# Kernel tuning notes

Hardware: AMD Instinct MI355X
Metric: run time of the kernel (lower is better)

## Reference

```python
import jax, jax.numpy as jnp
import numpy as np

B, S, D = 2, 2048, 2048
NH, NKV = 32, 8
HD = D // NH           # 64
GS = NH // NKV         # 4
ROPE_BASE = 10000.0


def _rope_tables(seq_len, head_dim, base):
    inv_freq = 1.0 / (base ** (jnp.arange(head_dim // 2, dtype=jnp.float32) / (head_dim // 2)))
    angles = jnp.arange(seq_len, dtype=jnp.float32)[:, None] * inv_freq[None, :]  # [S, HD/2]
    angles = jnp.concatenate([angles, angles], axis=-1)                            # [S, HD]
    return jnp.cos(angles), jnp.sin(angles)


def _apply_rope(x, cos, sin):
    # x: [B, H, S, HD]
    hd = x.shape[-1]
    x1, x2 = x[..., : hd // 2], x[..., hd // 2 :]
    rotated = jnp.concatenate([-x2, x1], axis=-1)
    return (x * cos[None, None] + rotated * sin[None, None]).astype(x.dtype)


def setup_inputs() -> dict:
    key = jax.random.key(0)
    ks = jax.random.split(key, 5)
    scale = 0.02
    return {
        "x": jax.random.normal(ks[0], (B, S, D), dtype=jnp.float32),
        "Wq": jax.random.normal(ks[1], (D, D), dtype=jnp.float32) * scale,
        "Wk": jax.random.normal(ks[2], (D, NKV * HD), dtype=jnp.float32) * scale,
        "Wv": jax.random.normal(ks[3], (D, NKV * HD), dtype=jnp.float32) * scale,
        "Wo": jax.random.normal(ks[4], (D, D), dtype=jnp.float32) * scale,
    }


def reference(x, Wq, Wk, Wv, Wo):
    b, n, _ = x.shape
    cos, sin = _rope_tables(n, HD, ROPE_BASE)

    q = (x @ Wq).reshape(b, n, NH, HD).transpose(0, 2, 1, 3)    # [B, NH, S, HD]
    k = (x @ Wk).reshape(b, n, NKV, HD).transpose(0, 2, 1, 3)   # [B, NKV, S, HD]
    v = (x @ Wv).reshape(b, n, NKV, HD).transpose(0, 2, 1, 3)

    q = _apply_rope(q, cos, sin)
    k = _apply_rope(k, cos, sin)

    # GQA head sharing: repeat_interleave KV groups to full head count
    k = jnp.repeat(k, GS, axis=1)   # [B, NH, S, HD]
    v = jnp.repeat(v, GS, axis=1)

    scores = jnp.einsum("bhqd,bhkd->bhqk", q, k)                # [B, NH, S, S]
    causal = jnp.triu(jnp.ones((n, n), dtype=bool), k=1)
    scores = jnp.where(causal[None, None], -jnp.inf, scores)
    weights = jax.nn.softmax(scores / jnp.sqrt(jnp.float32(HD)), axis=-1)

    ctx = jnp.einsum("bhqk,bhkd->bhqd", weights, v)             # [B, NH, S, HD]
    ctx = ctx.transpose(0, 2, 1, 3).reshape(b, n, D)
    return ctx @ Wo
```

## Files before the change

kernel.cpp:

```cpp
#include <hip/hip_runtime.h>

typedef __bf16 bf16;
typedef __attribute__((ext_vector_type(8))) __bf16 bf16x8;
typedef __attribute__((ext_vector_type(4))) float f32x4;
typedef __attribute__((ext_vector_type(4))) short s16x4;

#define S_LEN 2048
#define D_MODEL 2048
#define NHEADS 32
#define NKVH 8
#define HDIM 64
#define BATCH 2

__device__ __forceinline__ void async_cp16(const bf16* g, bf16* l) {
    __builtin_amdgcn_global_load_lds(
        (const __attribute__((address_space(1))) unsigned int*)g,
        (__attribute__((address_space(3))) unsigned int*)l, 16, 0, 0);
}

__global__ void preproc(const float* __restrict__ x,
                        const float* __restrict__ Wq, const float* __restrict__ Wk,
                        const float* __restrict__ Wv, const float* __restrict__ Wo,
                        bf16* __restrict__ X16, bf16* __restrict__ WqT, bf16* __restrict__ WkT,
                        bf16* __restrict__ WvT, bf16* __restrict__ WoT) {
    __shared__ float tile[32][33];
    const int tid = threadIdx.x;
    int bid = blockIdx.x;
    if (bid < 8192) {
        int i = bid * 256 + tid;
        float4 f = ((const float4*)x)[i];
        union { bf16 h[4]; uint2 u; } t;
        t.h[0] = (bf16)f.x; t.h[1] = (bf16)f.y; t.h[2] = (bf16)f.z; t.h[3] = (bf16)f.w;
        ((uint2*)X16)[i] = t.u;
        return;
    }
    int l = bid - 8192;
    const float* W; bf16* Wt; int N, bx, by;
    const int K = 2048;
    if (l < 4096)      {            W = Wq; Wt = WqT; N = 2048; bx = l & 63; by = l >> 6; }
    else if (l < 5120) { l -= 4096; W = Wk; Wt = WkT; N = 512;  bx = l & 15; by = l >> 4; }
    else if (l < 6144) { l -= 5120; W = Wv; Wt = WvT; N = 512;  bx = l & 15; by = l >> 4; }
    else               { l -= 6144; W = Wo; Wt = WoT; N = 2048; bx = l & 63; by = l >> 6; }
    const int kt = by * 32, nt = bx * 32;
    const int tx = tid & 31, ty = tid >> 5;
    #pragma unroll
    for (int i = 0; i < 32; i += 8)
        tile[ty + i][tx] = W[(size_t)(kt + ty + i) * N + nt + tx];
    __syncthreads();
    #pragma unroll
    for (int i = 0; i < 32; i += 8)
        Wt[(size_t)(nt + ty + i) * K + kt + tx] = (bf16)tile[tx][ty + i];
}

template <bool OUT_BF16>
__global__ __launch_bounds__(256) void gemm_bt(const bf16* __restrict__ A,
                                               const bf16* __restrict__ Bt,
                                               void* __restrict__ Cv,
                                               int M, int N, int K) {
    __shared__ __align__(16) bf16 As[128 * 64];
    __shared__ __align__(16) bf16 Bs[128 * 64];

    const int tid  = threadIdx.x;
    const int wave = tid >> 6;
    const int lane = tid & 63;
    const int l16  = lane & 15;
    const int quad = lane >> 4;
    const int wrow = (wave >> 1) * 64;
    const int wcol = (wave & 1) * 64;
    const int m0 = blockIdx.y * 128;
    const int n0 = blockIdx.x * 128;

    const int krow = lane >> 3;
    const int kc   = (lane & 7) ^ krow;
    const bf16* gA = A  + (size_t)(m0 + wave * 32 + krow) * K + kc * 8;
    const bf16* gB = Bt + (size_t)(n0 + wave * 32 + krow) * K + kc * 8;
    bf16* lA = &As[wave * 2048];
    bf16* lB = &Bs[wave * 2048];
    const size_t rstep = (size_t)8 * K;

    const int sw = l16 & 7;

    f32x4 acc[4][4];
    #pragma unroll
    for (int mi = 0; mi < 4; ++mi)
        #pragma unroll
        for (int ni = 0; ni < 4; ++ni)
            acc[mi][ni] = (f32x4){0.f, 0.f, 0.f, 0.f};

    for (int k0 = 0; k0 < K; k0 += 64) {
        __syncthreads();
        async_cp16(gA,             lA);
        async_cp16(gA +     rstep, lA + 512);
        async_cp16(gA + 2 * rstep, lA + 1024);
        async_cp16(gA + 3 * rstep, lA + 1536);
        async_cp16(gB,             lB);
        async_cp16(gB +     rstep, lB + 512);
        async_cp16(gB + 2 * rstep, lB + 1024);
        async_cp16(gB + 3 * rstep, lB + 1536);
        gA += 64; gB += 64;
        __syncthreads();

        #pragma unroll
        for (int kk = 0; kk < 2; ++kk) {
            bf16x8 af[4], bfr[4];
            #pragma unroll
            for (int mi = 0; mi < 4; ++mi)
                af[mi] = *(const bf16x8*)&As[(wrow + mi * 16 + l16) * 64 + (((kk * 4 + quad) ^ sw) * 8)];
            #pragma unroll
            for (int ni = 0; ni < 4; ++ni)
                bfr[ni] = *(const bf16x8*)&Bs[(wcol + ni * 16 + l16) * 64 + (((kk * 4 + quad) ^ sw) * 8)];
            #pragma unroll
            for (int mi = 0; mi < 4; ++mi)
                #pragma unroll
                for (int ni = 0; ni < 4; ++ni)
                    acc[mi][ni] = __builtin_amdgcn_mfma_f32_16x16x32_bf16(af[mi], bfr[ni], acc[mi][ni], 0, 0, 0);
        }
    }

    #pragma unroll
    for (int mi = 0; mi < 4; ++mi) {
        #pragma unroll
        for (int ni = 0; ni < 4; ++ni) {
            #pragma unroll
            for (int r = 0; r < 4; ++r) {
                size_t row = (size_t)(m0 + wrow + mi * 16 + quad * 4 + r);
                size_t col = (size_t)(n0 + wcol + ni * 16 + l16);
                if (OUT_BF16) ((bf16*)Cv)[row * N + col] = (bf16)acc[mi][ni][r];
                else          ((float*)Cv)[row * N + col] = acc[mi][ni][r];
            }
        }
    }
}

#define BUF1 16384

#define VMW(n) asm volatile("s_waitcnt vmcnt(" #n ")" ::: "memory")
#define BAR __builtin_amdgcn_s_barrier()

#define STAGE_A0(BUFOFF) do { \
    async_cp16(pa00, As + (BUFOFF) + la00); \
    async_cp16(pa01, As + (BUFOFF) + la01); \
    pa00 += 64; pa01 += 64; } while (0)
#define STAGE_A1(BUFOFF) do { \
    async_cp16(pa10, As + (BUFOFF) + la10); \
    async_cp16(pa11, As + (BUFOFF) + la11); \
    pa10 += 64; pa11 += 64; } while (0)
#define STAGE_B0(BUFOFF) do { \
    async_cp16(pb00, Bs + (BUFOFF) + lb00); \
    async_cp16(pb01, Bs + (BUFOFF) + lb01); \
    pb00 += 64; pb01 += 64; } while (0)
#define STAGE_B1(BUFOFF) do { \
    async_cp16(pb10, Bs + (BUFOFF) + lb10); \
    async_cp16(pb11, Bs + (BUFOFF) + lb11); \
    pb10 += 64; pb11 += 64; } while (0)

#define READ_A(QM, BUFOFF) do { \
    _Pragma("unroll") \
    for (int m_ = 0; m_ < 4; ++m_) { \
        const int row_ = wr * 128 + (QM) * 64 + m_ * 16 + l16; \
        af[m_][0] = *(const bf16x8*)&As[(BUFOFF) + row_ * 64 + ((quad ^ sw8) * 8)]; \
        af[m_][1] = *(const bf16x8*)&As[(BUFOFF) + row_ * 64 + (((4 + quad) ^ sw8) * 8)]; \
    } } while (0)

#define READ_B(QN, BUFOFF, BV) do { \
    _Pragma("unroll") \
    for (int n_ = 0; n_ < 2; ++n_) { \
        const int row_ = wc * 64 + (QN) * 32 + n_ * 16 + l16; \
        BV[n_][0] = *(const bf16x8*)&Bs[(BUFOFF) + row_ * 64 + ((quad ^ sw8) * 8)]; \
        BV[n_][1] = *(const bf16x8*)&Bs[(BUFOFF) + row_ * 64 + (((4 + quad) ^ sw8) * 8)]; \
    } } while (0)

#define MFMA_Q(QM, QN, BV) do { \
    _Pragma("unroll") \
    for (int kk_ = 0; kk_ < 2; ++kk_) \
        _Pragma("unroll") \
        for (int m_ = 0; m_ < 4; ++m_) \
            _Pragma("unroll") \
            for (int n_ = 0; n_ < 2; ++n_) \
                acc[(QM) * 4 + m_][(QN) * 2 + n_] = __builtin_amdgcn_mfma_f32_16x16x32_bf16( \
                    af[m_][kk_], BV[n_][kk_], acc[(QM) * 4 + m_][(QN) * 2 + n_], 0, 0, 0); \
    } while (0)

#define SYNCM(QM, QN, BV) do { \
    BAR; \
    __builtin_amdgcn_s_setprio(1); \
    MFMA_Q(QM, QN, BV); \
    __builtin_amdgcn_s_setprio(0); } while (0)

#define TILE_S(CUR) do { \
    READ_A(0, CUR); READ_B(0, CUR, bfr0);             SYNCM(0, 0, bfr0); BAR; \
    STAGE_A0(CUR); STAGE_B0(CUR); READ_B(1, CUR, bfr1); SYNCM(0, 1, bfr1); BAR; \
    STAGE_B1(CUR); READ_A(1, CUR);                    SYNCM(1, 0, bfr0); BAR; \
    STAGE_A1(CUR);                                    SYNCM(1, 1, bfr1); VMW(8); BAR; } while (0)

#define TILE_N(CUR, W) do { \
    READ_A(0, CUR); READ_B(0, CUR, bfr0); SYNCM(0, 0, bfr0); BAR; \
    READ_B(1, CUR, bfr1);                 SYNCM(0, 1, bfr1); BAR; \
    READ_A(1, CUR);                       SYNCM(1, 0, bfr0); BAR; \
                                          SYNCM(1, 1, bfr1); W; BAR; } while (0)

template <bool OUT_BF16>
__global__ __launch_bounds__(512, 2) void gemm256(const bf16* __restrict__ A,
                                                  const bf16* __restrict__ Bt,
                                                  void* __restrict__ Cv,
                                                  int N, int K) {
    __shared__ __align__(16) bf16 As[2 * 256 * 64];
    __shared__ __align__(16) bf16 Bs[2 * 256 * 64];

    const int tid  = threadIdx.x;
    const int w    = tid >> 6;
    const int lane = tid & 63;
    const int l16  = lane & 15;
    const int quad = lane >> 4;
    const int sw8  = l16 & 7;
    const int wr   = w >> 2;
    const int wc   = w & 3;

    const int nbx  = N >> 8;
    const int nwg  = gridDim.x;
    const int orig = blockIdx.x;
    const int wg   = (orig & 7) * (nwg >> 3) + (orig >> 3);
    const int n0   = (wg % nbx) * 256;
    const int m0   = (wg / nbx) * 256;

    const int krow = lane >> 3;
    const int kc   = (lane & 7) ^ krow;

    const bf16* pa00 = A + (size_t)(m0 +   0 + w * 8 + krow) * K + kc * 8;
    const bf16* pa01 = A + (size_t)(m0 + 128 + w * 8 + krow) * K + kc * 8;
    const bf16* pa10 = A + (size_t)(m0 +  64 + w * 8 + krow) * K + kc * 8;
    const bf16* pa11 = A + (size_t)(m0 + 192 + w * 8 + krow) * K + kc * 8;
    const int brow0 = (w >> 2) * 64 + (w & 3) * 8 + krow;
    const bf16* pb00 = Bt + (size_t)(n0 +       brow0) * K + kc * 8;
    const bf16* pb01 = Bt + (size_t)(n0 + 128 + brow0) * K + kc * 8;
    const bf16* pb10 = Bt + (size_t)(n0 +  32 + brow0) * K + kc * 8;
    const bf16* pb11 = Bt + (size_t)(n0 + 160 + brow0) * K + kc * 8;

    const int la00 = w * 512;
    const int la01 = 8192 + w * 512;
    const int la10 = 4096 + w * 512;
    const int la11 = 12288 + w * 512;
    const int lbb  = ((w >> 2) * 64 + (w & 3) * 8) * 64;
    const int lb00 = lbb;
    const int lb01 = 8192 + lbb;
    const int lb10 = 2048 + lbb;
    const int lb11 = 10240 + lbb;

    f32x4 acc[8][4];
    #pragma unroll
    for (int i = 0; i < 8; ++i)
        #pragma unroll
        for (int j = 0; j < 4; ++j) acc[i][j] = (f32x4){0.f, 0.f, 0.f, 0.f};

    bf16x8 af[4][2];
    bf16x8 bfr0[2][2];
    bf16x8 bfr1[2][2];

    STAGE_A0(0); STAGE_B0(0); STAGE_B1(0); STAGE_A1(0);
    STAGE_A0(BUF1); STAGE_B0(BUF1); STAGE_B1(BUF1); STAGE_A1(BUF1);
    VMW(8);
    BAR;

    const int NITER = K >> 6;
    for (int it = 0; it < (NITER - 2) >> 1; ++it) {
        TILE_S(0);
        TILE_S(BUF1);
    }
    TILE_N(0, VMW(0));
    TILE_N(BUF1, );

    #pragma unroll
    for (int mi = 0; mi < 8; ++mi)
        #pragma unroll
        for (int ni = 0; ni < 4; ++ni)
            #pragma unroll
            for (int r = 0; r < 4; ++r) {
                size_t row = (size_t)(m0 + wr * 128 + mi * 16 + quad * 4 + r);
                size_t col = (size_t)(n0 + wc * 64 + ni * 16 + l16);
                if (OUT_BF16) ((bf16*)Cv)[row * N + col] = (bf16)acc[mi][ni][r];
                else          ((float*)Cv)[row * N + col] = acc[mi][ni][r];
            }
}

__global__ void rope_tv(const bf16* __restrict__ QKV,
                        bf16* __restrict__ Qr, bf16* __restrict__ Kr,
                        bf16* __restrict__ Vt) {
    __shared__ bf16 tl[32][33];
    const int tid = threadIdx.x;
    const int bid = blockIdx.x;
    const float LC = 0.28782313662425572f;
    const float QS = 0.18033688011112042f;
    if (bid < 20480) {
        const int QN = BATCH * S_LEN * NHEADS * 32;
        int idx = bid * 256 + tid;
        if (idx < QN) {
            int j = idx & 31, hh = (idx >> 5) & 31, s = (idx >> 10) & 2047, bb = idx >> 21;
            size_t src = ((size_t)(bb * S_LEN + s)) * 3072 + hh * HDIM + j;
            float x1 = (float)QKV[src], x2 = (float)QKV[src + 32];
            float ang = (float)s * __expf(-(float)j * LC);
            float sn, cs; sincosf(ang, &sn, &cs);
            size_t dst = ((size_t)((bb * NHEADS + hh) * S_LEN + s)) * HDIM + j;
            Qr[dst]      = (bf16)((x1 * cs - x2 * sn) * QS);
            Qr[dst + 32] = (bf16)((x2 * cs + x1 * sn) * QS);
        } else {
            int t = idx - QN;
            int j = t & 31, hh = (t >> 5) & 7, s = (t >> 8) & 2047, bb = t >> 19;
            size_t src = ((size_t)(bb * S_LEN + s)) * 3072 + 2048 + hh * HDIM + j;
            float x1 = (float)QKV[src], x2 = (float)QKV[src + 32];
            float ang = (float)s * __expf(-(float)j * LC);
            float sn, cs; sincosf(ang, &sn, &cs);
            size_t dst = ((size_t)((bb * NKVH + hh) * S_LEN + s)) * HDIM + j;
            Kr[dst]      = (bf16)(x1 * cs - x2 * sn);
            Kr[dst + 32] = (bf16)(x2 * cs + x1 * sn);
        }
        return;
    }
    int l = bid - 20480;
    int s0 = (l & 63) * 32;
    int d0 = ((l >> 6) & 1) * 32;
    int z  = l >> 7;
    int bb = z >> 3, hh = z & 7;
    int tx = tid & 31, ty = tid >> 5;
    #pragma unroll
    for (int i = 0; i < 32; i += 8)
        tl[ty + i][tx] = QKV[((size_t)(bb * S_LEN + s0 + ty + i)) * 3072 + 2560 + hh * 64 + d0 + tx];
    __syncthreads();
    #pragma unroll
    for (int i = 0; i < 32; i += 8)
        Vt[((size_t)z * 64 + d0 + ty + i) * S_LEN + s0 + tx] = tl[tx][ty + i];
}

__global__ __launch_bounds__(256, 3) void attn_kernel(const bf16* __restrict__ Q,
                                                      const bf16* __restrict__ K,
                                                      const bf16* __restrict__ Vt,
                                                      bf16* __restrict__ Ctx) {
    __shared__ __align__(16) bf16 KsL[128 * 64];
    __shared__ __align__(16) bf16 VtL[64 * 128];

    static const signed char QTAB[16] = {15,14,13,12, 10,11,8,9, 5,4,7,6, 0,1,2,3};
    const int bx = blockIdx.x;
    const int qt = QTAB[((bx >> 8) << 2) | ((bx >> 6) & 3)];
    const int bh = bx & 63;
    const int b  = bh >> 5;
    const int h  = bh & 31;
    const int kvh = h >> 2;
    const int tid = threadIdx.x;
    const int wave = tid >> 6;
    const int lane = tid & 63;
    const int l16  = lane & 15;
    const int quad = lane >> 4;

    const bf16* Qb = Q  + ((size_t)(b * NHEADS + h)) * S_LEN * HDIM;
    const bf16* Kb = K  + ((size_t)(b * NKVH + kvh)) * S_LEN * HDIM;
    const bf16* Vb = Vt + ((size_t)(b * NKVH + kvh)) * HDIM * S_LEN;

    const int q0 = qt * 128;

    bf16x8 aq[2][2];
    #pragma unroll
    for (int qf = 0; qf < 2; ++qf)
        #pragma unroll
        for (int ks = 0; ks < 2; ++ks)
            aq[qf][ks] = *(const bf16x8*)(Qb + (size_t)(q0 + wave * 32 + qf * 16 + l16) * HDIM + ks * 32 + quad * 8);

    f32x4 O[2][4];
    float M0 = -1e30f, M1 = -1e30f;
    float l0 = 0.f, l1 = 0.f;
    #pragma unroll
    for (int qf = 0; qf < 2; ++qf)
        #pragma unroll
        for (int df = 0; df < 4; ++df) O[qf][df] = (f32x4){0.f,0.f,0.f,0.f};

    const int krow = lane >> 3, kslot = lane & 7;
    const int kc   = kslot ^ (krow & 7);
    const int vslot = lane & 15, vsub = lane >> 4;

    #pragma unroll 1
    for (int kt = 0; kt <= qt; ++kt) {
        const int k0 = kt * 128;
        __syncthreads();
        #pragma unroll
        for (int j = 0; j < 4; ++j) {
            int rbase = (wave * 4 + j) * 8;
            async_cp16(Kb + (size_t)(k0 + rbase + krow) * HDIM + kc * 8, &KsL[rbase * 64]);
            int d0 = (wave * 4 + j) * 4;
            int vrow = d0 + vsub;
            int vc = vslot ^ (vrow & 15);
            async_cp16(Vb + (size_t)vrow * S_LEN + k0 + vc * 8, &VtL[d0 * 128]);
        }
        __syncthreads();

        f32x4 sc[2][8];
        #pragma unroll
        for (int kf = 0; kf < 8; ++kf) {
            sc[0][kf] = (f32x4){0.f,0.f,0.f,0.f};
            sc[1][kf] = (f32x4){0.f,0.f,0.f,0.f};
            #pragma unroll
            for (int ks = 0; ks < 2; ++ks) {
                bf16x8 bk = *(const bf16x8*)&KsL[(kf * 16 + l16) * 64 + (((ks * 4 + quad) ^ (l16 & 7)) * 8)];
                sc[0][kf] = __builtin_amdgcn_mfma_f32_16x16x32_bf16(bk, aq[0][ks], sc[0][kf], 0, 0, 0);
                sc[1][kf] = __builtin_amdgcn_mfma_f32_16x16x32_bf16(bk, aq[1][ks], sc[1][kf], 0, 0, 0);
            }
        }

        if (kt == qt) {
            #pragma unroll
            for (int kf = 0; kf < 8; ++kf)
                #pragma unroll
                for (int r = 0; r < 4; ++r) {
                    int key = kf * 16 + quad * 4 + r;
                    int qi0 = wave * 32 + l16;
                    if (key > qi0)      sc[0][kf][r] = -1e30f;
                    if (key > qi0 + 16) sc[1][kf][r] = -1e30f;
                }
        }

        float mx0 = sc[0][0][0], mx1 = sc[1][0][0];
        #pragma unroll
        for (int kf = 0; kf < 8; ++kf)
            #pragma unroll
            for (int r = 0; r < 4; ++r) {
                mx0 = fmaxf(mx0, sc[0][kf][r]);
                mx1 = fmaxf(mx1, sc[1][kf][r]);
            }
        mx0 = fmaxf(mx0, __shfl_xor(mx0, 16)); mx0 = fmaxf(mx0, __shfl_xor(mx0, 32));
        mx1 = fmaxf(mx1, __shfl_xor(mx1, 16)); mx1 = fmaxf(mx1, __shfl_xor(mx1, 32));

        if (!__all((mx0 <= M0 + 8.0f) && (mx1 <= M1 + 8.0f))) {
            float Mn0 = fmaxf(M0, mx0), Mn1 = fmaxf(M1, mx1);
            float a0 = __builtin_amdgcn_exp2f(M0 - Mn0);
            float a1 = __builtin_amdgcn_exp2f(M1 - Mn1);
            M0 = Mn0; M1 = Mn1;
            l0 *= a0; l1 *= a1;
            #pragma unroll
            for (int r = 0; r < 4; ++r) {
                float aO0 = __shfl(a0, quad * 4 + r);
                float aO1 = __shfl(a1, quad * 4 + r);
                #pragma unroll
                for (int df = 0; df < 4; ++df) {
                    O[0][df][r] *= aO0;
                    O[1][df][r] *= aO1;
                }
            }
        }

        #pragma unroll
        for (int kf = 0; kf < 8; ++kf)
            #pragma unroll
            for (int r = 0; r < 4; ++r) {
                float e0 = __builtin_amdgcn_exp2f(sc[0][kf][r] - M0); sc[0][kf][r] = e0; l0 += e0;
                float e1 = __builtin_amdgcn_exp2f(sc[1][kf][r] - M1); sc[1][kf][r] = e1; l1 += e1;
            }

        #pragma unroll
        for (int kf = 0; kf < 8; ++kf) {
            union { bf16 hh[4]; s16x4 s4; } p0, p1;
            #pragma unroll
            for (int r = 0; r < 4; ++r) {
                p0.hh[r] = (bf16)sc[0][kf][r];
                p1.hh[r] = (bf16)sc[1][kf][r];
            }
            #pragma unroll
            for (int df = 0; df < 4; ++df) {
                s16x4 bv = *(const s16x4*)&VtL[(df * 16 + l16) * 128 +
                                               (((kf * 2 + (quad >> 1)) ^ l16) * 8) + (quad & 1) * 4];
                O[0][df] = __builtin_amdgcn_mfma_f32_16x16x16bf16_1k(p0.s4, bv, O[0][df], 0, 0, 0);
                O[1][df] = __builtin_amdgcn_mfma_f32_16x16x16bf16_1k(p1.s4, bv, O[1][df], 0, 0, 0);
            }
        }
    }

    l0 += __shfl_xor(l0, 16); l0 += __shfl_xor(l0, 32);
    l1 += __shfl_xor(l1, 16); l1 += __shfl_xor(l1, 32);
    #pragma unroll
    for (int r = 0; r < 4; ++r) {
        float inv0 = 1.0f / __shfl(l0, quad * 4 + r);
        float inv1 = 1.0f / __shfl(l1, quad * 4 + r);
        size_t row0 = (size_t)b * S_LEN + q0 + wave * 32 + quad * 4 + r;
        bf16* dst0 = Ctx + row0 * D_MODEL + h * HDIM;
        bf16* dst1 = dst0 + (size_t)16 * D_MODEL;
        #pragma unroll
        for (int df = 0; df < 4; ++df) {
            dst0[df * 16 + l16] = (bf16)(O[0][df][r] * inv0);
            dst1[df * 16 + l16] = (bf16)(O[1][df][r] * inv1);
        }
    }
}

extern "C" void kernel_launch(void* const* d_in, const int* in_sizes, int n_in,
                              void* d_out, int out_size, void* d_ws, size_t ws_size,
                              hipStream_t stream) {
    const float* x  = (const float*)d_in[0];
    const float* Wq = (const float*)d_in[1];
    const float* Wk = (const float*)d_in[2];
    const float* Wv = (const float*)d_in[3];
    const float* Wo = (const float*)d_in[4];

    char* p = (char*)d_ws;
    bf16* X16 = (bf16*)p; p += (size_t)4096 * 2048 * 2;
    bf16* WqT = (bf16*)p; p += (size_t)2048 * 2048 * 2;
    bf16* WkT = (bf16*)p; p += (size_t)512 * 2048 * 2;
    bf16* WvT = (bf16*)p; p += (size_t)512 * 2048 * 2;
    bf16* WoT = (bf16*)p; p += (size_t)2048 * 2048 * 2;
    bf16* QKV = (bf16*)p; p += (size_t)4096 * 3072 * 2;
    bf16* Qr  = (bf16*)p; p += (size_t)4096 * 2048 * 2;
    bf16* Kr  = (bf16*)p; p += (size_t)4096 * 512 * 2;
    bf16* Vt  = (bf16*)p; p += (size_t)16 * 64 * 2048 * 2;
    bf16* Ctx = QKV;

    preproc<<<18432, 256, 0, stream>>>(x, Wq, Wk, Wv, Wo, X16, WqT, WkT, WvT, WoT);

    gemm256<true><<<dim3(192), 512, 0, stream>>>(X16, WqT, (void*)QKV, 3072, 2048);

    rope_tv<<<22528, 256, 0, stream>>>(QKV, Qr, Kr, Vt);

    attn_kernel<<<1024, 256, 0, stream>>>(Qr, Kr, Vt, Ctx);

    gemm_bt<false><<<dim3(16, 32), 256, 0, stream>>>(Ctx, WoT, d_out, 4096, 2048, 2048);
}
```

Measured before the change: 293.0 us.

## Fuse RoPE into QKV GEMM epilogue and drop lazy softmax rescale

The QKV projection GEMM now applies RoPE (and the Q scale) in its epilogue, writing rotated Q and K straight into head-major buffers and writing only the V columns to the QKV buffer. The separate rope kernel becomes a V-only transpose kernel. This removes a full read and write of Q/K through global memory plus one kernel launch, at the cost of sincos work and scattered 2-byte stores inside the GEMM epilogue. The attention kernel also drops the thresholded lazy rescale branch and always rescales the running output, which adds work every iteration but removes a wave-wide vote and a branch.

```diff
diff --git a/kernel.cpp b/kernel.cpp
--- a/kernel.cpp
+++ b/kernel.cpp
@@ -199,11 +199,12 @@
     READ_A(1, CUR);                       SYNCM(1, 0, bfr0); BAR; \
                                           SYNCM(1, 1, bfr1); W; BAR; } while (0)
 
-template <bool OUT_BF16>
-__global__ __launch_bounds__(512, 2) void gemm256(const bf16* __restrict__ A,
-                                                  const bf16* __restrict__ Bt,
-                                                  void* __restrict__ Cv,
-                                                  int N, int K) {
+__global__ __launch_bounds__(512, 2) void gemm_qkv_rope(const bf16* __restrict__ A,
+                                                        const bf16* __restrict__ Bt,
+                                                        bf16* __restrict__ QKV,
+                                                        bf16* __restrict__ Qr,
+                                                        bf16* __restrict__ Kr) {
+    const int N = 3072, K = 2048;
     __shared__ __align__(16) bf16 As[2 * 256 * 64];
     __shared__ __align__(16) bf16 Bs[2 * 256 * 64];
 
@@ -269,58 +270,56 @@
     TILE_N(0, VMW(0));
     TILE_N(BUF1, );
 
-    #pragma unroll
-    for (int mi = 0; mi < 8; ++mi)
-        #pragma unroll
-        for (int ni = 0; ni < 4; ++ni)
-            #pragma unroll
-            for (int r = 0; r < 4; ++r) {
-                size_t row = (size_t)(m0 + wr * 128 + mi * 16 + quad * 4 + r);
-                size_t col = (size_t)(n0 + wc * 64 + ni * 16 + l16);
-                if (OUT_BF16) ((bf16*)Cv)[row * N + col] = (bf16)acc[mi][ni][r];
-                else          ((float*)Cv)[row * N + col] = acc[mi][ni][r];
-            }
-}
-
-__global__ void rope_tv(const bf16* __restrict__ QKV,
-                        bf16* __restrict__ Qr, bf16* __restrict__ Kr,
-                        bf16* __restrict__ Vt) {
-    __shared__ bf16 tl[32][33];
-    const int tid = threadIdx.x;
-    const int bid = blockIdx.x;
     const float LC = 0.28782313662425572f;
     const float QS = 0.18033688011112042f;
-    if (bid < 20480) {
-        const int QN = BATCH * S_LEN * NHEADS * 32;
-        int idx = bid * 256 + tid;
-        if (idx < QN) {
-            int j = idx & 31, hh = (idx >> 5) & 31, s = (idx >> 10) & 2047, bb = idx >> 21;
-            size_t src = ((size_t)(bb * S_LEN + s)) * 3072 + hh * HDIM + j;
-            float x1 = (float)QKV[src], x2 = (float)QKV[src + 32];
-            float ang = (float)s * __expf(-(float)j * LC);
-            float sn, cs; sincosf(ang, &sn, &cs);
-            size_t dst = ((size_t)((bb * NHEADS + hh) * S_LEN + s)) * HDIM + j;
-            Qr[dst]      = (bf16)((x1 * cs - x2 * sn) * QS);
-            Qr[dst + 32] = (bf16)((x2 * cs + x1 * sn) * QS);
-        } else {
-            int t = idx - QN;
-            int j = t & 31, hh = (t >> 5) & 7, s = (t >> 8) & 2047, bb = t >> 19;
-            size_t src = ((size_t)(bb * S_LEN + s)) * 3072 + 2048 + hh * HDIM + j;
-            float x1 = (float)QKV[src], x2 = (float)QKV[src + 32];
-            float ang = (float)s * __expf(-(float)j * LC);
-            float sn, cs; sincosf(ang, &sn, &cs);
-            size_t dst = ((size_t)((bb * NKVH + hh) * S_LEN + s)) * HDIM + j;
-            Kr[dst]      = (bf16)(x1 * cs - x2 * sn);
-            Kr[dst + 32] = (bf16)(x2 * cs + x1 * sn);
-        }
-        return;
-    }
-    int l = bid - 20480;
-    int s0 = (l & 63) * 32;
-    int d0 = ((l >> 6) & 1) * 32;
-    int z  = l >> 7;
+    const int c0 = n0 + wc * 64;
+    const int rbase = m0 + wr * 128;
+
+    if (c0 < 2560) {
+        const bool isQ = c0 < 2048;
+        const float scale = isQ ? QS : 1.0f;
+        const int hh = isQ ? (c0 >> 6) : ((c0 - 2048) >> 6);
+        const int HN = isQ ? NHEADS : NKVH;
+        bf16* const base = isQ ? Qr : Kr;
+        const float f0 = __expf(-(float)(l16) * LC);
+        const float f1 = __expf(-(float)(l16 + 16) * LC);
+        #pragma unroll
+        for (int mi = 0; mi < 8; ++mi) {
+            #pragma unroll
+            for (int r = 0; r < 4; ++r) {
+                int row = rbase + mi * 16 + quad * 4 + r;
+                int bb = row >> 11, s = row & 2047;
+                bf16* dst = base + (((size_t)(bb * HN + hh) * S_LEN + s) << 6);
+                float sn0, cs0, sn1, cs1;
+                sincosf((float)s * f0, &sn0, &cs0);
+                sincosf((float)s * f1, &sn1, &cs1);
+                float x10 = acc[mi][0][r], x20 = acc[mi][2][r];
+                float x11 = acc[mi][1][r], x21 = acc[mi][3][r];
+                dst[l16]      = (bf16)((x10 * cs0 - x20 * sn0) * scale);
+                dst[l16 + 32] = (bf16)((x20 * cs0 + x10 * sn0) * scale);
+                dst[l16 + 16] = (bf16)((x11 * cs1 - x21 * sn1) * scale);
+                dst[l16 + 48] = (bf16)((x21 * cs1 + x11 * sn1) * scale);
+            }
+        }
+    } else {
+        #pragma unroll
+        for (int mi = 0; mi < 8; ++mi)
+            #pragma unroll
+            for (int ni = 0; ni < 4; ++ni)
+                #pragma unroll
+                for (int r = 0; r < 4; ++r) {
+                    size_t row = (size_t)(rbase + mi * 16 + quad * 4 + r);
+                    QKV[row * 3072 + c0 + ni * 16 + l16] = (bf16)acc[mi][ni][r];
+                }
+    }
+}
+
+__global__ void transpose_v(const bf16* __restrict__ QKV, bf16* __restrict__ Vt) {
+    __shared__ bf16 tl[32][33];
+    int z = blockIdx.z;
+    int s0 = blockIdx.x * 32, d0 = blockIdx.y * 32;
     int bb = z >> 3, hh = z & 7;
-    int tx = tid & 31, ty = tid >> 5;
+    int tx = threadIdx.x, ty = threadIdx.y;
     #pragma unroll
     for (int i = 0; i < 32; i += 8)
         tl[ty + i][tx] = QKV[((size_t)(bb * S_LEN + s0 + ty + i)) * 3072 + 2560 + hh * 64 + d0 + tx];
@@ -426,21 +425,20 @@
         mx0 = fmaxf(mx0, __shfl_xor(mx0, 16)); mx0 = fmaxf(mx0, __shfl_xor(mx0, 32));
         mx1 = fmaxf(mx1, __shfl_xor(mx1, 16)); mx1 = fmaxf(mx1, __shfl_xor(mx1, 32));
 
-        if (!__all((mx0 <= M0 + 8.0f) && (mx1 <= M1 + 8.0f))) {
-            float Mn0 = fmaxf(M0, mx0), Mn1 = fmaxf(M1, mx1);
-            float a0 = __builtin_amdgcn_exp2f(M0 - Mn0);
-            float a1 = __builtin_amdgcn_exp2f(M1 - Mn1);
-            M0 = Mn0; M1 = Mn1;
-            l0 *= a0; l1 *= a1;
-            #pragma unroll
-            for (int r = 0; r < 4; ++r) {
-                float aO0 = __shfl(a0, quad * 4 + r);
-                float aO1 = __shfl(a1, quad * 4 + r);
-                #pragma unroll
-                for (int df = 0; df < 4; ++df) {
-                    O[0][df][r] *= aO0;
-                    O[1][df][r] *= aO1;
-                }
+        float Mn0 = fmaxf(M0, mx0), Mn1 = fmaxf(M1, mx1);
+        float a0 = __builtin_amdgcn_exp2f(M0 - Mn0);
+        float a1 = __builtin_amdgcn_exp2f(M1 - Mn1);
+        M0 = Mn0; M1 = Mn1;
+        l0 *= a0; l1 *= a1;
+
+        #pragma unroll
+        for (int r = 0; r < 4; ++r) {
+            float aO0 = __shfl(a0, quad * 4 + r);
+            float aO1 = __shfl(a1, quad * 4 + r);
+            #pragma unroll
+            for (int df = 0; df < 4; ++df) {
+                O[0][df][r] *= aO0;
+                O[1][df][r] *= aO1;
             }
         }
 
@@ -510,9 +508,9 @@
 
     preproc<<<18432, 256, 0, stream>>>(x, Wq, Wk, Wv, Wo, X16, WqT, WkT, WvT, WoT);
 
-    gemm256<true><<<dim3(192), 512, 0, stream>>>(X16, WqT, (void*)QKV, 3072, 2048);
-
-    rope_tv<<<22528, 256, 0, stream>>>(QKV, Qr, Kr, Vt);
+    gemm_qkv_rope<<<dim3(192), 512, 0, stream>>>(X16, WqT, QKV, Qr, Kr);
+
+    transpose_v<<<dim3(64, 2, 16), dim3(32, 8), 0, stream>>>(QKV, Vt);
 
     attn_kernel<<<1024, 256, 0, stream>>>(Qr, Kr, Vt, Ctx);
 
```

After: 310.7 us. 1.06x slower.
